# Performance work log

Hardware: AMD Instinct MI355X
Metric: run time of the kernel (lower is better)

The kernel has to match this reference:

```python
import jax, jax.numpy as jnp
import numpy as np

B, N = 4, 20                        # batch, qubits
L = int(np.ceil(np.log2(N)))        # 5 layers, one 4x4 generator each


def setup_inputs():
    key = jax.random.key(0)
    k1, k2, k3, k4 = jax.random.split(key, 4)
    psi_re = jax.random.normal(k1, (B, 2 ** N), dtype=jnp.float32)
    psi_im = jax.random.normal(k2, (B, 2 ** N), dtype=jnp.float32)
    nrm = jnp.sqrt(jnp.sum(psi_re ** 2 + psi_im ** 2, axis=1, keepdims=True))
    psi_re, psi_im = psi_re / nrm, psi_im / nrm   # normalized quantum state
    H_re = jax.random.normal(k3, (L, 4, 4), dtype=jnp.float32)
    H_im = jax.random.normal(k4, (L, 4, 4), dtype=jnp.float32)
    return {"psi_re": psi_re, "psi_im": psi_im, "H_re": H_re, "H_im": H_im}


def _make_unitary(A):
    # torch.matrix_exp(A - A^H): expm of an anti-Hermitian generator via eigh
    G = A - A.conj().T
    w, V = jnp.linalg.eigh(-1j * G)            # G = i * Hermitian
    return (V * jnp.exp(1j * w)) @ V.conj().T  # expm(G), unitary


def _apply_gate(T, U4, axes):
    # contract 4x4 gate (reshaped [2,2,2,2]) onto two qubit axes of tensor T
    T = jnp.tensordot(U4, T, axes=((2, 3), axes))
    return jnp.moveaxis(T, (0, 1), axes)


def _gate_pairs(nq):
    pairs = [(2 * i, 2 * i + 1) for i in range(nq // 2)]
    if nq > 2:
        pairs += [(2 * i + 1, (2 * i + 2) % nq) for i in range(nq // 2)]
    return pairs


def _forward(psi_re, psi_im, H_re, H_im):
    psi = (psi_re + 1j * psi_im).astype(jnp.complex64).reshape((B,) + (2,) * N)
    H = (H_re + 1j * H_im).astype(jnp.complex64)
    state, is_dm, nq = psi, False, N
    for layer in range(L):
        U = _make_unitary(H[layer]).reshape(2, 2, 2, 2)
        Uc = U.conj()
        # _2local_conv: brick pattern of the same 2-qubit gate
        for (a, b) in _gate_pairs(nq):
            state = _apply_gate(state, U, (1 + a, 1 + b))
            if is_dm:  # density matrix: also apply U* on bra axes
                state = _apply_gate(state, Uc, (1 + nq + a, 1 + nq + b))
        # _2local_pool: measuring qubits 0..nq//2-1 with index shifting removes
        # the even-indexed qubits -> partial trace over them
        if nq >= 2:
            traced = [2 * i for i in range(nq // 2)]
            kept = [q for q in range(nq) if q not in traced]
            t, k = len(traced), len(kept)
            if is_dm:
                perm = (0,) + tuple(1 + q for q in kept) + tuple(1 + q for q in traced) \
                     + tuple(1 + nq + q for q in kept) + tuple(1 + nq + q for q in traced)
                r = jnp.transpose(state, perm).reshape(B, 2 ** k, 2 ** t, 2 ** k, 2 ** t)
                state = jnp.einsum('bitjt->bij', r).reshape((B,) + (2,) * k + (2,) * k)
            else:
                perm = (0,) + tuple(1 + q for q in traced) + tuple(1 + q for q in kept)
                p = jnp.transpose(state, perm).reshape(B, 2 ** t, 2 ** k)
                state = jnp.einsum('bti,btj->bij', p, p.conj()).reshape((B,) + (2,) * k + (2,) * k)
                is_dm = True
            nq = k
    # final state.measure(0): reduced 1-qubit density matrix, take P(outcome 0)
    r = state.reshape(B, 2, 2 ** (nq - 1), 2, 2 ** (nq - 1))
    rho0 = jnp.einsum('birjr->bij', r)
    return rho0[:, 0, 0].real


def reference(psi_re, psi_im, H_re, H_im):
    return _forward(psi_re, psi_im, H_re, H_im)
```

## Files before the change

kernel.cpp:

```cpp
#include <hip/hip_runtime.h>
#include <math.h>


typedef float cpx __attribute__((ext_vector_type(2)));

__device__ __forceinline__ cpx mkc(float x, float y) { cpx r; r.x = x; r.y = y; return r; }

__device__ __forceinline__ cpx cmul(cpx a, cpx b) {
  cpx r = a.xx * b;
  return __builtin_elementwise_fma(mkc(-a.y, a.y), b.yx, r);
}
__device__ __forceinline__ cpx cmadd(cpx acc, cpx a, cpx b) {
  acc = __builtin_elementwise_fma(a.xx, b, acc);
  return __builtin_elementwise_fma(mkc(-a.y, a.y), b.yx, acc);
}
__device__ __forceinline__ cpx cmaddc(cpx acc, cpx a, cpx b) {
  acc = __builtin_elementwise_fma(a.xx, mkc(b.x, -b.y), acc);
  return __builtin_elementwise_fma(a.yy, b.yx, acc);
}

__device__ __forceinline__ int pad(int e) { return e + (e >> 4); }
__device__ __forceinline__ int ins(int x, int p) {
  return ((x >> p) << (p + 1)) | (x & ((1 << p) - 1));
}

__device__ __forceinline__ void gate4(cpx& v0, cpx& v1, cpx& v2, cpx& v3,
                                      const cpx (&U)[16]) {
  cpx n0 = cmul(U[0], v0);  n0 = cmadd(n0, U[1], v1);  n0 = cmadd(n0, U[2], v2);  n0 = cmadd(n0, U[3], v3);
  cpx n1 = cmul(U[4], v0);  n1 = cmadd(n1, U[5], v1);  n1 = cmadd(n1, U[6], v2);  n1 = cmadd(n1, U[7], v3);
  cpx n2 = cmul(U[8], v0);  n2 = cmadd(n2, U[9], v1);  n2 = cmadd(n2, U[10], v2); n2 = cmadd(n2, U[11], v3);
  cpx n3 = cmul(U[12], v0); n3 = cmadd(n3, U[13], v1); n3 = cmadd(n3, U[14], v2); n3 = cmadd(n3, U[15], v3);
  v0 = n0; v1 = n1; v2 = n2; v3 = n3;
}

template <int NG>
__device__ __forceinline__ void gate16n(cpx (&v)[16], const cpx (&U)[16]) {
#pragma unroll
  for (int g = 0; g < 4; g++)
    gate4(v[g * 4 + 0], v[g * 4 + 1], v[g * 4 + 2], v[g * 4 + 3], U);
#pragma unroll
  for (int lo = 0; lo < 4; lo++)
    gate4(v[lo], v[lo + 4], v[lo + 8], v[lo + 12], U);
  if (NG == 3) {
#pragma unroll
    for (int b3 = 0; b3 < 2; b3++)
#pragma unroll
      for (int b0 = 0; b0 < 2; b0++) {
        int j = b3 * 8 + b0;
        gate4(v[j], v[j + 2], v[j + 4], v[j + 6], U);
      }
  }
}

__device__ __forceinline__ void apply_gate_tile13(cpx* t, const cpx (&U)[16],
                                                  int pa, int pb, int tid) {
  int p0 = pa < pb ? pa : pb;
  int p1 = pa < pb ? pb : pa;
  int m0 = (1 << p0) - 1, m1 = (1 << p1) - 1;
  int ia = 1 << pa, ib = 1 << pb;
#pragma unroll
  for (int g = tid; g < 2048; g += 512) {
    int idx = ((g & ~m0) << 1) | (g & m0);
    idx = ((idx & ~m1) << 1) | (idx & m1);
    int e0 = pad(idx), e1 = pad(idx | ib), e2 = pad(idx | ia), e3 = pad(idx | ia | ib);
    cpx v0 = t[e0], v1 = t[e1], v2 = t[e2], v3 = t[e3];
    gate4(v0, v1, v2, v3, U);
    t[e0] = v0; t[e1] = v1; t[e2] = v2; t[e3] = v3;
  }
}

template <int NG>
__device__ __forceinline__ void phase4_f(cpx* t, const cpx (&U)[16],
                                         int q0, int q1, int q2, int q3,
                                         int o0, int o1, int o2, int o3, int tid) {
  int idx = ins(ins(ins(ins(tid, q0), q1), q2), q3);
  cpx v[16];
#pragma unroll
  for (int j = 0; j < 16; j++) {
    int off = ((j & 1) ? o0 : 0) + ((j & 2) ? o1 : 0) + ((j & 4) ? o2 : 0) + ((j & 8) ? o3 : 0);
    v[j] = t[pad(idx + off)];
  }
  gate16n<NG>(v, U);
#pragma unroll
  for (int j = 0; j < 16; j++) {
    int off = ((j & 1) ? o0 : 0) + ((j & 2) ? o1 : 0) + ((j & 4) ? o2 : 0) + ((j & 8) ? o3 : 0);
    t[pad(idx + off)] = v[j];
  }
}

template <int NG>
__device__ __forceinline__ void phase4_pool(cpx* w, const cpx (&U)[16],
                                            int a_lo, int a_hi, int c_lo, int c_hi,
                                            int o0, int o1, int o2, int o3, int tid) {
  int uu = tid & 7, ss = (tid >> 3) & 7, t_lo = tid >> 6;
  int u = ins(ins(uu, a_lo), a_hi);
  int s = ins(ins(ss, c_lo), c_hi);
  int base = t_lo * 1120 + s * 35 + u;
  cpx v[16];
#pragma unroll
  for (int j = 0; j < 16; j++) {
    int off = ((j & 1) ? o0 : 0) + ((j & 2) ? o1 : 0) + ((j & 4) ? o2 : 0) + ((j & 8) ? o3 : 0);
    v[j] = w[base + off];
  }
  gate16n<NG>(v, U);
#pragma unroll
  for (int j = 0; j < 16; j++) {
    int off = ((j & 1) ? o0 : 0) + ((j & 2) ? o1 : 0) + ((j & 4) ? o2 : 0) + ((j & 8) ? o3 : 0);
    w[base + off] = v[j];
  }
}

__device__ __forceinline__ void pool_p3(cpx* w, const cpx (&U)[16], int tid) {
#pragma unroll
  for (int it = 0; it < 2; it++) {
    int h = tid + it * 512;
    int uu = h & 7, ss = (h >> 3) & 15, t_lo = h >> 7;
    int base = t_lo * 1120 + (ss << 1) * 35 + (uu << 2);
    cpx v[8];
    v[0] = w[base];      v[1] = w[base + 1];
    v[4] = w[base + 2];  v[5] = w[base + 3];
    v[2] = w[base + 35]; v[3] = w[base + 36];
    v[6] = w[base + 37]; v[7] = w[base + 38];
    gate4(v[0], v[1], v[2], v[3], U);
    gate4(v[4], v[5], v[6], v[7], U);
    gate4(v[0], v[2], v[4], v[6], U);
    gate4(v[1], v[3], v[5], v[7], U);
    w[base] = v[0];      w[base + 1] = v[1];
    w[base + 2] = v[4];  w[base + 3] = v[5];
    w[base + 35] = v[2]; w[base + 36] = v[3];
    w[base + 37] = v[6]; w[base + 38] = v[7];
  }
}

__device__ __forceinline__ cpx expm16(const float* __restrict__ Hre,
                                      const float* __restrict__ Him,
                                      int l, int l16) {
  int r = l16 >> 2, c = l16 & 3;
  double tr = (double)Hre[l * 16 + r * 4 + c] - (double)Hre[l * 16 + c * 4 + r];
  double ti = (double)Him[l * 16 + r * 4 + c] + (double)Him[l * 16 + c * 4 + r];
  double a = sqrt(tr * tr + ti * ti);
  a += __shfl_xor(a, 1, 16);
  a += __shfl_xor(a, 2, 16);
  double nrm = fmax(a, __shfl_xor(a, 4, 16));
  nrm = fmax(nrm, __shfl_xor(nrm, 8, 16));
  int s = 0;
  while (nrm > 0.25 && s < 60) { nrm *= 0.5; s++; }
  double sc = ldexp(1.0, -s);
  tr *= sc; ti *= sc;
  double id = (r == c) ? 1.0 : 0.0;
  double er = id, ei = 0.0, pr = id, pi = 0.0;
  for (int k = 1; k <= 16; k++) {
    double qr = 0.0, qi = 0.0;
#pragma unroll
    for (int m = 0; m < 4; m++) {
      double pmr = __shfl(pr, r * 4 + m, 16);
      double pmi = __shfl(pi, r * 4 + m, 16);
      double tmr = __shfl(tr, m * 4 + c, 16);
      double tmi = __shfl(ti, m * 4 + c, 16);
      qr = fma(pmr, tmr, fma(-pmi, tmi, qr));
      qi = fma(pmr, tmi, fma(pmi, tmr, qi));
    }
    double inv = 1.0 / (double)k;
    pr = qr * inv; pi = qi * inv;
    er += pr; ei += pi;
  }
  for (int it = 0; it < s; it++) {
    double qr = 0.0, qi = 0.0;
#pragma unroll
    for (int m = 0; m < 4; m++) {
      double amr = __shfl(er, r * 4 + m, 16);
      double ami = __shfl(ei, r * 4 + m, 16);
      double bmr = __shfl(er, m * 4 + c, 16);
      double bmi = __shfl(ei, m * 4 + c, 16);
      qr = fma(amr, bmr, fma(-ami, bmi, qr));
      qi = fma(amr, bmi, fma(ami, bmr, qi));
    }
    er = qr; ei = qi;
  }
  return mkc((float)er, (float)ei);
}

__global__ __launch_bounds__(512, 4) void l0_pass1(const float* __restrict__ pre,
                                                   const float* __restrict__ pim,
                                                   const float* __restrict__ Hre,
                                                   const float* __restrict__ Him,
                                                   cpx* __restrict__ Umat,
                                                   cpx* __restrict__ state,
                                                   float4* __restrict__ accz) {
  extern __shared__ cpx tile[];
  __shared__ cpx Ush[16];
  int tid = threadIdx.x;
  int bid = blockIdx.x;
  int b = bid >> 7, hi = bid & 127;
  size_t base = ((size_t)b << 20) | ((size_t)hi << 13);
  if (tid < 32) accz[(bid << 5) | tid] = make_float4(0.f, 0.f, 0.f, 0.f);
  for (int e4 = tid; e4 < 2048; e4 += 512) {
    int e = e4 << 2;
    float4 re = *(const float4*)&pre[base + e];
    float4 im = *(const float4*)&pim[base + e];
    int d = pad(e);
    tile[d] = mkc(re.x, im.x);
    tile[d + 1] = mkc(re.y, im.y);
    tile[d + 2] = mkc(re.z, im.z);
    tile[d + 3] = mkc(re.w, im.w);
  }
  {
    int wv = tid >> 6, g16 = (tid & 63) >> 4, l16 = tid & 15;
    int layer = (wv == 0) ? g16 : ((wv == 1 && g16 == 0) ? 4 : -1);
    if (layer == 0 || (bid == 0 && layer > 0)) {
      cpx ue = expm16(Hre, Him, layer, l16);
      if (layer == 0) Ush[l16] = ue;
      if (bid == 0) Umat[layer * 16 + l16] = ue;
    }
  }
  __syncthreads();
  cpx U[16];
#pragma unroll
  for (int k = 0; k < 16; k++) U[k] = Ush[k];
  phase4_f<3>(tile, U, 0, 1, 2, 3, 1, 2, 4, 8, tid);            __syncthreads();
  phase4_f<3>(tile, U, 4, 5, 6, 7, 16, 32, 64, 128, tid);       __syncthreads();
  phase4_f<3>(tile, U, 8, 9, 10, 11, 256, 512, 1024, 2048, tid);__syncthreads();
  phase4_f<2>(tile, U, 3, 4, 7, 8, 8, 16, 128, 256, tid);       __syncthreads();
  int hifix = ((hi & 1) << 16) | (((hi >> 1) & 1) << 6) | (((hi >> 2) & 1) << 17)
            | (((hi >> 3) & 1) << 5) | (((hi >> 4) & 1) << 18) | (((hi >> 5) & 1) << 7)
            | (((hi >> 6) & 1) << 19);
  size_t dbase = ((size_t)b << 20) | (unsigned)hifix;
  for (int e4 = tid; e4 < 2048; e4 += 512) {
    int le = e4;
    int d = ((le & 1) << 2) | (((le >> 1) & 1) << 3) | (((le >> 2) & 1) << 8)
          | (((le >> 3) & 1) << 12) | (((le >> 4) & 1) << 10) | (((le >> 5) & 1) << 13)
          | (((le >> 6) & 1) << 9) | (((le >> 7) & 1) << 14) | (((le >> 8) & 1) << 11)
          | (((le >> 9) & 1) << 15) | (((le >> 10) & 1) << 4);
    int src = pad(e4 << 2);
    cpx x0 = tile[src], x1 = tile[src + 1], x2 = tile[src + 2], x3 = tile[src + 3];
    float4* dst = (float4*)&state[dbase + d];
    dst[0] = make_float4(x0.x, x0.y, x1.x, x1.y);
    dst[1] = make_float4(x2.x, x2.y, x3.x, x3.y);
  }
}

__global__ __launch_bounds__(512, 4) void l0_pass2(const cpx* __restrict__ Umat,
                                                   cpx* __restrict__ state) {
  extern __shared__ cpx tile[];
  int tid = threadIdx.x;
  int bid = blockIdx.x;
  int b = bid >> 7, mid = bid & 127;
  size_t base = ((size_t)b << 20) | ((size_t)mid << 8);
  cpx U[16];
#pragma unroll
  for (int k = 0; k < 16; k++) U[k] = Umat[k];
  for (int f = tid; f < 4096; f += 512) {
    int run = f >> 7, idx = f & 127;
    size_t a = base + ((size_t)run << 15) + ((size_t)idx << 1);
    float4 v = *(const float4*)&state[a];
    int d = pad(run * 256 + idx * 2);
    tile[d] = mkc(v.x, v.y);
    tile[d + 1] = mkc(v.z, v.w);
  }
  __syncthreads();
  phase4_f<3>(tile, U, 4, 6, 9, 10, 16, 512, 64, 1024, tid);    __syncthreads();
  phase4_f<3>(tile, U, 5, 7, 11, 12, 32, 2048, 128, 4096, tid); __syncthreads();
  phase4_f<2>(tile, U, 4, 5, 8, 10, 256, 16, 1024, 32, tid);    __syncthreads();
  apply_gate_tile13(tile, U, 0, 12, tid);                       __syncthreads();
  for (int f = tid; f < 4096; f += 512) {
    int run = f >> 7, idx = f & 127;
    size_t a = base + ((size_t)run << 15) + ((size_t)idx << 1);
    int d = pad(run * 256 + idx * 2);
    cpx x0 = tile[d], x1 = tile[d + 1];
    *(float4*)&state[a] = make_float4(x0.x, x0.y, x1.x, x1.y);
  }
}

__global__ __launch_bounds__(512, 4) void pool_l1(const cpx* __restrict__ Umat,
                                                  const cpx* __restrict__ state,
                                                  float* __restrict__ accbuf) {
  extern __shared__ cpx w[];
  int tid = threadIdx.x;
  int bid = blockIdx.x;
  int b = bid >> 7, thi = bid & 127;
  size_t base = ((size_t)b << 20) | ((size_t)thi << 13);
  cpx U[16];
#pragma unroll
  for (int k = 0; k < 16; k++) U[k] = Umat[16 + k];
  for (int f = tid; f < 4096; f += 512) {
    int e = f << 1;
    float4 v = *(const float4*)&state[base + e];
    int u = (((e >> 8) & 1) << 1) | (((e >> 9) & 1) << 2) | (((e >> 4) & 1) << 3) | (((e >> 5) & 1) << 4);
    int s = ((e >> 2) & 1) | (((e >> 10) & 1) << 1) | (((e >> 11) & 1) << 2)
          | (((e >> 6) & 1) << 3) | (((e >> 7) & 1) << 4);
    int t = ((e >> 1) & 1) | (((e >> 3) & 1) << 1) | (((e >> 12) & 1) << 2);
    int c = t * 1120 + s * 35 + u;
    w[c] = mkc(v.x, v.y);
    w[c + 1] = mkc(v.z, v.w);
  }
  __syncthreads();
  phase4_pool<3>(w, U, 3, 4, 3, 4, 8, 280, 16, 560, tid); __syncthreads();
  phase4_pool<3>(w, U, 1, 2, 1, 2, 2, 70, 4, 140, tid);   __syncthreads();
  pool_p3(w, U, tid);                                     __syncthreads();
  phase4_pool<2>(w, U, 0, 3, 2, 4, 140, 8, 560, 1, tid);  __syncthreads();
  int wv = tid >> 6, lane = tid & 63;
  int u0 = (lane >> 3) << 2, v0 = (lane & 7) << 2;
  cpx acc[4][4];
#pragma unroll
  for (int i = 0; i < 4; i++)
#pragma unroll
    for (int j = 0; j < 4; j++) acc[i][j] = mkc(0.f, 0.f);
  {
    int tb = wv * 1120;
#pragma unroll 4
    for (int s = 0; s < 32; s++) {
      int row = tb + s * 35;
      cpx x[4], y[4];
#pragma unroll
      for (int i = 0; i < 4; i++) { x[i] = w[row + u0 + i]; y[i] = w[row + v0 + i]; }
#pragma unroll
      for (int i = 0; i < 4; i++)
#pragma unroll
        for (int j = 0; j < 4; j++) acc[i][j] = cmaddc(acc[i][j], x[i], y[j]);
    }
  }
  __syncthreads();
  if (wv > 0) {
#pragma unroll
    for (int i = 0; i < 4; i++)
#pragma unroll
      for (int j = 0; j < 4; j++)
        w[(wv - 1) * 1024 + (u0 + i) * 32 + (v0 + j)] = acc[i][j];
  }
  __syncthreads();
  if (wv == 0) {
    float* dst = accbuf + ((size_t)((b << 3) | (thi & 7)) << 11);
#pragma unroll
    for (int i = 0; i < 4; i++)
#pragma unroll
      for (int j = 0; j < 4; j++) {
        cpx a = acc[i][j];
#pragma unroll
        for (int k = 0; k < 7; k++) {
          cpx o = w[k * 1024 + (u0 + i) * 32 + (v0 + j)];
          a.x += o.x; a.y += o.y;
        }
        int off = (((u0 + i) << 5) | (v0 + j)) << 1;
        atomicAdd(dst + off, a.x);
        atomicAdd(dst + off + 1, a.y);
      }
  }
}

__global__ __launch_bounds__(256) void finish(const cpx* __restrict__ Umat,
                                              const float4* __restrict__ accv,
                                              float* __restrict__ out) {
  __shared__ cpx rho[1024];
  __shared__ cpx r3s[64];
  __shared__ cpx r4s[16];
  int tid = threadIdx.x;
  int b = blockIdx.x;
  float4* rf = (float4*)rho;
  for (int f = tid; f < 512; f += 256) {
    float4 acc = make_float4(0.f, 0.f, 0.f, 0.f);
#pragma unroll
    for (int r = 0; r < 8; r++) {
      float4 v = accv[(size_t)((b << 3) | r) * 512 + f];
      acc.x += v.x; acc.y += v.y; acc.z += v.z; acc.w += v.w;
    }
    rf[f] = acc;
  }
  __syncthreads();

  cpx U[16], Uc[16];
#pragma unroll
  for (int k = 0; k < 16; k++) { U[k] = Umat[32 + k]; Uc[k] = mkc(U[k].x, -U[k].y); }
  const int gl2[4][2] = {{4,3},{2,1},{3,2},{1,0}};
#pragma unroll
  for (int gi = 0; gi < 4; gi++) {
    int pa = gl2[gi][0], pb = gl2[gi][1];
    int p0 = pa < pb ? pa : pb, p1 = pa < pb ? pb : pa;
    int m0 = (1 << p0) - 1, m1 = (1 << p1) - 1;
    int ia = 1 << pa, ib = 1 << pb;
    {
      int j = tid >> 3, g = tid & 7;
      int idx = ((g & ~m0) << 1) | (g & m0);
      idx = ((idx & ~m1) << 1) | (idx & m1);
      cpx v0 = rho[idx * 32 + j], v1 = rho[(idx | ib) * 32 + j];
      cpx v2 = rho[(idx | ia) * 32 + j], v3 = rho[(idx | ia | ib) * 32 + j];
      gate4(v0, v1, v2, v3, U);
      rho[idx * 32 + j] = v0; rho[(idx | ib) * 32 + j] = v1;
      rho[(idx | ia) * 32 + j] = v2; rho[(idx | ia | ib) * 32 + j] = v3;
    }
    __syncthreads();
    {
      int i = tid >> 3, g = tid & 7;
      int idx = ((g & ~m0) << 1) | (g & m0);
      idx = ((idx & ~m1) << 1) | (idx & m1);
      cpx v0 = rho[i * 32 + idx], v1 = rho[i * 32 + (idx | ib)];
      cpx v2 = rho[i * 32 + (idx | ia)], v3 = rho[i * 32 + (idx | ia | ib)];
      gate4(v0, v1, v2, v3, Uc);
      rho[i * 32 + idx] = v0; rho[i * 32 + (idx | ib)] = v1;
      rho[i * 32 + (idx | ia)] = v2; rho[i * 32 + (idx | ia | ib)] = v3;
    }
    __syncthreads();
  }
  if (tid < 64) {
    int u = tid >> 3, v = tid & 7;
    cpx acc = mkc(0.f, 0.f);
#pragma unroll
    for (int s = 0; s < 4; s++) {
      int iu = ((s >> 1) << 4) | ((u >> 2) << 3) | ((s & 1) << 2) | (((u >> 1) & 1) << 1) | (u & 1);
      int iv = ((s >> 1) << 4) | ((v >> 2) << 3) | ((s & 1) << 2) | (((v >> 1) & 1) << 1) | (v & 1);
      cpx x = rho[iu * 32 + iv];
      acc.x += x.x; acc.y += x.y;
    }
    r3s[u * 8 + v] = acc;
  }
  __syncthreads();

#pragma unroll
  for (int k = 0; k < 16; k++) { U[k] = Umat[48 + k]; Uc[k] = mkc(U[k].x, -U[k].y); }
  const int gl3[2][2] = {{2,1},{1,0}};
#pragma unroll
  for (int gi = 0; gi < 2; gi++) {
    int pa = gl3[gi][0], pb = gl3[gi][1];
    int p0 = pa < pb ? pa : pb, p1 = pa < pb ? pb : pa;
    int m0 = (1 << p0) - 1, m1 = (1 << p1) - 1;
    int ia = 1 << pa, ib = 1 << pb;
    if (tid < 16) {
      int j = tid >> 1, g = tid & 1;
      int idx = ((g & ~m0) << 1) | (g & m0);
      idx = ((idx & ~m1) << 1) | (idx & m1);
      cpx v0 = r3s[idx * 8 + j], v1 = r3s[(idx | ib) * 8 + j];
      cpx v2 = r3s[(idx | ia) * 8 + j], v3 = r3s[(idx | ia | ib) * 8 + j];
      gate4(v0, v1, v2, v3, U);
      r3s[idx * 8 + j] = v0; r3s[(idx | ib) * 8 + j] = v1;
      r3s[(idx | ia) * 8 + j] = v2; r3s[(idx | ia | ib) * 8 + j] = v3;
    }
    __syncthreads();
    if (tid < 16) {
      int i = tid >> 1, g = tid & 1;
      int idx = ((g & ~m0) << 1) | (g & m0);
      idx = ((idx & ~m1) << 1) | (idx & m1);
      cpx v0 = r3s[i * 8 + idx], v1 = r3s[i * 8 + (idx | ib)];
      cpx v2 = r3s[i * 8 + (idx | ia)], v3 = r3s[i * 8 + (idx | ia | ib)];
      gate4(v0, v1, v2, v3, Uc);
      r3s[i * 8 + idx] = v0; r3s[i * 8 + (idx | ib)] = v1;
      r3s[i * 8 + (idx | ia)] = v2; r3s[i * 8 + (idx | ia | ib)] = v3;
    }
    __syncthreads();
  }
  if (tid < 16) {
    int u = tid >> 2, v = tid & 3;
    cpx acc = mkc(0.f, 0.f);
#pragma unroll
    for (int s = 0; s < 2; s++) {
      cpx x = r3s[((s << 2) | u) * 8 + ((s << 2) | v)];
      acc.x += x.x; acc.y += x.y;
    }
    r4s[u * 4 + v] = acc;
  }
  __syncthreads();

#pragma unroll
  for (int k = 0; k < 16; k++) { U[k] = Umat[64 + k]; Uc[k] = mkc(U[k].x, -U[k].y); }
  if (tid < 4) {
    int j = tid;
    cpx v0 = r4s[0 * 4 + j], v1 = r4s[1 * 4 + j], v2 = r4s[2 * 4 + j], v3 = r4s[3 * 4 + j];
    gate4(v0, v1, v2, v3, U);
    r4s[0 * 4 + j] = v0; r4s[1 * 4 + j] = v1; r4s[2 * 4 + j] = v2; r4s[3 * 4 + j] = v3;
  }
  __syncthreads();
  if (tid < 4) {
    int i = tid;
    cpx v0 = r4s[i * 4 + 0], v1 = r4s[i * 4 + 1], v2 = r4s[i * 4 + 2], v3 = r4s[i * 4 + 3];
    gate4(v0, v1, v2, v3, Uc);
    r4s[i * 4 + 0] = v0; r4s[i * 4 + 1] = v1; r4s[i * 4 + 2] = v2; r4s[i * 4 + 3] = v3;
  }
  __syncthreads();
  if (tid == 0) out[b] = r4s[0].x + r4s[10].x;
}

extern "C" void kernel_launch(void* const* d_in, const int* in_sizes, int n_in,
                              void* d_out, int out_size, void* d_ws, size_t ws_size,
                              hipStream_t stream) {
  const float* psi_re = (const float*)d_in[0];
  const float* psi_im = (const float*)d_in[1];
  const float* H_re = (const float*)d_in[2];
  const float* H_im = (const float*)d_in[3];
  float* out = (float*)d_out;

  char* ws = (char*)d_ws;
  cpx* Umat = (cpx*)ws;
  float* accb = (float*)(ws + 4096);
  cpx* state = (cpx*)(ws + ((size_t)1 << 19));

  const size_t LDS_L0 = 8704 * sizeof(cpx);
  const size_t LDS_POOL = 8960 * sizeof(cpx);

  hipLaunchKernelGGL(l0_pass1, dim3(512), dim3(512), LDS_L0, stream,
                     psi_re, psi_im, H_re, H_im, Umat, state, (float4*)accb);
  hipLaunchKernelGGL(l0_pass2, dim3(512), dim3(512), LDS_L0, stream,
                     (const cpx*)Umat, state);
  hipLaunchKernelGGL(pool_l1, dim3(512), dim3(512), LDS_POOL, stream,
                     (const cpx*)Umat, (const cpx*)state, accb);
  hipLaunchKernelGGL(finish, dim3(4), dim3(256), 0, stream,
                     (const cpx*)Umat, (const float4*)accb, out);
}
```

Before: 180.7 us.

## Replace atomic accumulation with per-block partials reduced in finish kernel

Measured after the change: 174.1 us. 1.04x faster.

```diff
diff --git a/kernel.cpp b/kernel.cpp
--- a/kernel.cpp
+++ b/kernel.cpp
@@ -185,15 +185,13 @@
                                                    const float* __restrict__ Hre,
                                                    const float* __restrict__ Him,
                                                    cpx* __restrict__ Umat,
-                                                   cpx* __restrict__ state,
-                                                   float4* __restrict__ accz) {
+                                                   cpx* __restrict__ state) {
   extern __shared__ cpx tile[];
   __shared__ cpx Ush[16];
   int tid = threadIdx.x;
   int bid = blockIdx.x;
   int b = bid >> 7, hi = bid & 127;
   size_t base = ((size_t)b << 20) | ((size_t)hi << 13);
-  if (tid < 32) accz[(bid << 5) | tid] = make_float4(0.f, 0.f, 0.f, 0.f);
   for (int e4 = tid; e4 < 2048; e4 += 512) {
     int e = e4 << 2;
     float4 re = *(const float4*)&pre[base + e];
@@ -273,7 +271,7 @@
 
 __global__ __launch_bounds__(512, 4) void pool_l1(const cpx* __restrict__ Umat,
                                                   const cpx* __restrict__ state,
-                                                  float* __restrict__ accbuf) {
+                                                  float4* __restrict__ partial) {
   extern __shared__ cpx w[];
   int tid = threadIdx.x;
   int bid = blockIdx.x;
@@ -320,30 +318,20 @@
     }
   }
   __syncthreads();
-  if (wv > 0) {
-#pragma unroll
-    for (int i = 0; i < 4; i++)
-#pragma unroll
-      for (int j = 0; j < 4; j++)
-        w[(wv - 1) * 1024 + (u0 + i) * 32 + (v0 + j)] = acc[i][j];
-  }
-  __syncthreads();
-  if (wv == 0) {
-    float* dst = accbuf + ((size_t)((b << 3) | (thi & 7)) << 11);
-#pragma unroll
-    for (int i = 0; i < 4; i++)
-#pragma unroll
-      for (int j = 0; j < 4; j++) {
-        cpx a = acc[i][j];
-#pragma unroll
-        for (int k = 0; k < 7; k++) {
-          cpx o = w[k * 1024 + (u0 + i) * 32 + (v0 + j)];
-          a.x += o.x; a.y += o.y;
-        }
-        int off = (((u0 + i) << 5) | (v0 + j)) << 1;
-        atomicAdd(dst + off, a.x);
-        atomicAdd(dst + off + 1, a.y);
-      }
+#pragma unroll
+  for (int i = 0; i < 4; i++)
+#pragma unroll
+    for (int j = 0; j < 4; j++)
+      w[wv * 1024 + (u0 + i) * 32 + (v0 + j)] = acc[i][j];
+  __syncthreads();
+  {
+    cpx s0 = mkc(0.f, 0.f), s1 = mkc(0.f, 0.f);
+#pragma unroll
+    for (int k = 0; k < 8; k++) {
+      s0 += w[k * 1024 + 2 * tid];
+      s1 += w[k * 1024 + 2 * tid + 1];
+    }
+    partial[((size_t)bid << 9) | tid] = make_float4(s0.x, s0.y, s1.x, s1.y);
   }
 }
 
@@ -358,9 +346,9 @@
   float4* rf = (float4*)rho;
   for (int f = tid; f < 512; f += 256) {
     float4 acc = make_float4(0.f, 0.f, 0.f, 0.f);
-#pragma unroll
-    for (int r = 0; r < 8; r++) {
-      float4 v = accv[(size_t)((b << 3) | r) * 512 + f];
+#pragma unroll 8
+    for (int h = 0; h < 128; h++) {
+      float4 v = accv[(size_t)(b * 128 + h) * 512 + f];
       acc.x += v.x; acc.y += v.y; acc.z += v.z; acc.w += v.w;
     }
     rf[f] = acc;
@@ -488,18 +476,18 @@
 
   char* ws = (char*)d_ws;
   cpx* Umat = (cpx*)ws;
-  float* accb = (float*)(ws + 4096);
-  cpx* state = (cpx*)(ws + ((size_t)1 << 19));
+  cpx* state = (cpx*)(ws + 4096);
+  float4* partial = (float4*)(ws + 4096 + ((size_t)1 << 25));
 
   const size_t LDS_L0 = 8704 * sizeof(cpx);
   const size_t LDS_POOL = 8960 * sizeof(cpx);
 
   hipLaunchKernelGGL(l0_pass1, dim3(512), dim3(512), LDS_L0, stream,
-                     psi_re, psi_im, H_re, H_im, Umat, state, (float4*)accb);
+                     psi_re, psi_im, H_re, H_im, Umat, state);
   hipLaunchKernelGGL(l0_pass2, dim3(512), dim3(512), LDS_L0, stream,
                      (const cpx*)Umat, state);
   hipLaunchKernelGGL(pool_l1, dim3(512), dim3(512), LDS_POOL, stream,
-                     (const cpx*)Umat, (const cpx*)state, accb);
+                     (const cpx*)Umat, (const cpx*)state, partial);
   hipLaunchKernelGGL(finish, dim3(4), dim3(256), 0, stream,
-                     (const cpx*)Umat, (const float4*)accb, out);
-}
+                     (const cpx*)Umat, (const float4*)partial, out);
+}
```
